# Performance work log

Hardware: AMD Instinct MI355X
Metric: run time of the kernel (lower is better)

## Reference

```python
import jax, jax.numpy as jnp
import numpy as np


def setup_inputs() -> dict:
    key = jax.random.key(0)
    k1, k2, k3, k4, k5 = jax.random.split(key, 5)
    B, C, G, H, W = 2, 64, 4, 64, 64
    CG = C * G            # 256 complex input channels (flattened)
    DQK = max(C // 8, 1)  # 8  query/key channels after gabor pooling
    scale = 1.0 / np.sqrt(CG)
    x = jax.random.normal(k1, (2, B, C, G, H, W), dtype=jnp.float32)
    wq = jax.random.normal(k2, (2, DQK, CG), dtype=jnp.float32) * scale
    wk = jax.random.normal(k3, (2, DQK, CG), dtype=jnp.float32) * scale
    wv = jax.random.normal(k4, (2, CG, CG), dtype=jnp.float32) * scale
    gamma = jax.random.normal(k5, (1,), dtype=jnp.float32) * 0.1
    return {"x": x, "wq": wq, "wk": wk, "wv": wv, "gamma": gamma}


def _cconv1x1(w, xr, xi):
    """Complex 1x1 conv: (wr+i wi)(xr+i xi). w: (2,O,Cin), x: (B,Cin,L)."""
    wr, wi = w[0], w[1]
    yr = jnp.einsum('oc,bcl->bol', wr, xr) - jnp.einsum('oc,bcl->bol', wi, xi)
    yi = jnp.einsum('oc,bcl->bol', wr, xi) + jnp.einsum('oc,bcl->bol', wi, xr)
    return yr, yi


def reference(x, wq, wk, wv, gamma):
    _, B, C, G, H, W = x.shape
    L = H * W
    xr = x[0].reshape(B, C * G, L)
    xi = x[1].reshape(B, C * G, L)
    # complex Q (B,d,L) / K (B,d,L)
    qr, qi = _cconv1x1(wq, xr, xi)
    kr, ki = _cconv1x1(wk, xr, xi)
    # energy = Q^H-free complex bmm: energy[b,l,m] = sum_d q[b,d,l] * k[b,d,m]
    er = jnp.einsum('bdl,bdm->blm', qr, kr) - jnp.einsum('bdl,bdm->blm', qi, ki)
    ei = jnp.einsum('bdl,bdm->blm', qr, ki) + jnp.einsum('bdl,bdm->blm', qi, kr)
    # magnitude-squared softmax over last axis -> real attention (B,L,L)
    att = jax.nn.softmax(er * er + ei * ei, axis=-1)
    # complex V (B,CG,L); out[b,c,m] = sum_l v[b,c,l] * att[b,m,l]
    vr, vi = _cconv1x1(wv, xr, xi)
    out_r = jnp.einsum('bcl,bml->bcm', vr, att)
    out_i = jnp.einsum('bcl,bml->bcm', vi, att)
    out = jnp.stack([out_r, out_i]).reshape(2, B, C, G, H, W)
    return gamma * out + x
```

## Files before the change

### kernel.cpp

```cpp
#include <hip/hip_runtime.h>
#include <cstdint>

constexpr int Bc  = 2;
constexpr int CGc = 256;
constexpr int Dc  = 8;
constexpr int Lc  = 4096;

typedef __attribute__((ext_vector_type(8))) short short8;
typedef __attribute__((ext_vector_type(4))) float floatx4;

__device__ inline unsigned short f2bf(float f) {
  union { float f; unsigned u; } v; v.f = f;
  unsigned r = v.u + 0x7fffu + ((v.u >> 16) & 1u);
  return (unsigned short)(r >> 16);
}
__device__ inline float bf2f(unsigned short h) {
  return __uint_as_float((unsigned)h << 16);
}

__global__ __launch_bounds__(256) void init_stats(float* __restrict__ p) {
  p[blockIdx.x * 256 + threadIdx.x] = 0.f;
}

__global__ __launch_bounds__(256) void wcat_pack(const float* __restrict__ wv,
                                                 unsigned short* __restrict__ Wcat) {
  const int i  = blockIdx.x * 256 + threadIdx.x;
  const int cc = i >> 9, k = i & 511;
  const int co = cc >> 8, c = cc & 255, ci = k >> 8, cin = k & 255;
  const float wr = wv[(size_t)c * CGc + cin];
  const float wi = wv[(size_t)(CGc + c) * CGc + cin];
  const float val = co == 0 ? (ci == 0 ? wr : -wi) : (ci == 0 ? wi : wr);
  Wcat[i] = f2bf(val);
}

__global__ __launch_bounds__(256) void xT_pack(const float* __restrict__ x,
                                               unsigned short* __restrict__ Xlk) {
  __shared__ float xs[64][65];
  const int tid = threadIdx.x;
  const int b   = blockIdx.z;
  const int l0  = blockIdx.x * 64;
  const int c0  = blockIdx.y * 64;
  const int lt  = tid & 63, r4 = tid >> 6;
#pragma unroll
  for (int p = 0; p < 16; ++p) {
    const int row  = p * 4 + r4;
    const int cin2 = c0 + row;
    const int comp = cin2 >> 8, cin = cin2 & 255;
    xs[row][lt] = x[((size_t)(comp * Bc + b) * CGc + cin) * Lc + l0 + lt];
  }
  __syncthreads();
#pragma unroll
  for (int p = 0; p < 16; ++p) {
    const int lr = p * 4 + r4;
    Xlk[((size_t)b * Lc + l0 + lr) * 512 + c0 + lt] = f2bf(xs[lt][lr]);
  }
}

__global__ __launch_bounds__(256) void qk_proj(const float* __restrict__ x,
                                               const float* __restrict__ wq,
                                               const float* __restrict__ wk,
                                               float* __restrict__ qout,
                                               float* __restrict__ kout) {
  __shared__ float ws[4 * Dc * CGc];
  const int tid = threadIdx.x;
  const int b   = blockIdx.y;
  for (int i = tid; i < 2 * Dc * CGc; i += 256) {
    ws[i]                 = wq[i];
    ws[2 * Dc * CGc + i]  = wk[i];
  }
  __syncthreads();
  const int d  = tid >> 5;
  const int ml = tid & 31;
  const int m  = blockIdx.x * 32 + ml;
  const float* xr = x + ((size_t)(0 * Bc + b) * CGc) * Lc + m;
  const float* xi = x + ((size_t)(1 * Bc + b) * CGc) * Lc + m;
  const float* wqr = ws + d * CGc;
  const float* wqi = ws + (Dc + d) * CGc;
  const float* wkr = ws + 2 * Dc * CGc + d * CGc;
  const float* wki = ws + 2 * Dc * CGc + (Dc + d) * CGc;
  float qer = 0.f, qei = 0.f, ker = 0.f, kei = 0.f;
#pragma unroll 4
  for (int cin = 0; cin < CGc; ++cin) {
    const float vr = xr[(size_t)cin * Lc];
    const float vi = xi[(size_t)cin * Lc];
    const float a1 = wqr[cin], b1 = wqi[cin];
    qer = fmaf(a1, vr, qer); qer = fmaf(-b1, vi, qer);
    qei = fmaf(a1, vi, qei); qei = fmaf(b1, vr, qei);
    const float a2 = wkr[cin], b2 = wki[cin];
    ker = fmaf(a2, vr, ker); ker = fmaf(-b2, vi, ker);
    kei = fmaf(a2, vi, kei); kei = fmaf(b2, vr, kei);
  }
  float* qp = qout + ((size_t)b * Lc + m) * 16;
  qp[d]     = qer;
  qp[8 + d] = qei;
  float* kp = kout + ((size_t)b * Lc + m) * 16;
  kp[d]     = ker;
  kp[8 + d] = kei;
}

__global__ __launch_bounds__(256) void qk_pack(const float* __restrict__ q,
                                               const float* __restrict__ k,
                                               unsigned short* __restrict__ Qcat,
                                               unsigned short* __restrict__ K1hi,
                                               unsigned short* __restrict__ K1lo,
                                               unsigned short* __restrict__ K2hi,
                                               unsigned short* __restrict__ K2lo) {
  const int r = blockIdx.x * 256 + threadIdx.x;
  {
    const float* qp = q + (size_t)r * 16;
    unsigned u[16];
#pragma unroll
    for (int t = 0; t < 8; ++t) {
      const float v0 = qp[2 * t], v1 = qp[2 * t + 1];
      const unsigned short h0 = f2bf(v0), h1 = f2bf(v1);
      u[t] = (unsigned)h0 | ((unsigned)h1 << 16);
      const unsigned short l0 = f2bf(v0 - bf2f(h0));
      const unsigned short l1 = f2bf(v1 - bf2f(h1));
      u[8 + t] = (unsigned)l0 | ((unsigned)l1 << 16);
    }
    uint4* dst = (uint4*)(Qcat + (size_t)r * 32);
    dst[0] = make_uint4(u[0], u[1], u[2], u[3]);
    dst[1] = make_uint4(u[4], u[5], u[6], u[7]);
    dst[2] = make_uint4(u[8], u[9], u[10], u[11]);
    dst[3] = make_uint4(u[12], u[13], u[14], u[15]);
  }
  {
    const float* kp = k + (size_t)r * 16;
    float k1[16], k2[16];
#pragma unroll
    for (int d = 0; d < 8; ++d) {
      const float kr = kp[d], ki = kp[8 + d];
      k1[d] = kr;  k1[8 + d] = -ki;
      k2[d] = ki;  k2[8 + d] = kr;
    }
    unsigned uh[8], ul[8];
#pragma unroll
    for (int t = 0; t < 8; ++t) {
      const unsigned short h0 = f2bf(k1[2 * t]), h1 = f2bf(k1[2 * t + 1]);
      uh[t] = (unsigned)h0 | ((unsigned)h1 << 16);
      const unsigned short l0 = f2bf(k1[2 * t] - bf2f(h0));
      const unsigned short l1 = f2bf(k1[2 * t + 1] - bf2f(h1));
      ul[t] = (unsigned)l0 | ((unsigned)l1 << 16);
    }
    uint4* dh = (uint4*)(K1hi + (size_t)r * 16);
    dh[0] = make_uint4(uh[0], uh[1], uh[2], uh[3]);
    dh[1] = make_uint4(uh[4], uh[5], uh[6], uh[7]);
    uint4* dl = (uint4*)(K1lo + (size_t)r * 16);
    dl[0] = make_uint4(ul[0], ul[1], ul[2], ul[3]);
    dl[1] = make_uint4(ul[4], ul[5], ul[6], ul[7]);
#pragma unroll
    for (int t = 0; t < 8; ++t) {
      const unsigned short h0 = f2bf(k2[2 * t]), h1 = f2bf(k2[2 * t + 1]);
      uh[t] = (unsigned)h0 | ((unsigned)h1 << 16);
      const unsigned short l0 = f2bf(k2[2 * t] - bf2f(h0));
      const unsigned short l1 = f2bf(k2[2 * t + 1] - bf2f(h1));
      ul[t] = (unsigned)l0 | ((unsigned)l1 << 16);
    }
    uint4* dh2 = (uint4*)(K2hi + (size_t)r * 16);
    dh2[0] = make_uint4(uh[0], uh[1], uh[2], uh[3]);
    dh2[1] = make_uint4(uh[4], uh[5], uh[6], uh[7]);
    uint4* dl2 = (uint4*)(K2lo + (size_t)r * 16);
    dl2[0] = make_uint4(ul[0], ul[1], ul[2], ul[3]);
    dl2[1] = make_uint4(ul[4], ul[5], ul[6], ul[7]);
  }
}

__global__ __launch_bounds__(256) void v_gemm(const unsigned short* __restrict__ Wcat,
                                              const unsigned short* __restrict__ Xlk,
                                              unsigned short* __restrict__ vbf) {
  __shared__ short As[128 * 64];
  __shared__ short Bs[64 * 64];
  const int tid  = threadIdx.x;
  const int b    = blockIdx.z;
  const int cc0  = blockIdx.x * 128;
  const int l0   = blockIdx.y * 64;
  const int wid  = tid >> 6, lane = tid & 63;
  const int wcc  = (wid >> 1) * 64;
  const int wl   = (wid & 1) * 32;
  const int lrow = lane & 15, quad = lane >> 4;
  floatx4 acc[4][2] = {};
  const unsigned short* wsrc = Wcat + (size_t)cc0 * 512;
  const unsigned short* xsrc = Xlk + ((size_t)b * Lc + l0) * 512;
  int s_off[4], g_off[4];
#pragma unroll
  for (int r = 0; r < 4; ++r) {
    const int idx = r * 256 + tid;
    const int row = idx >> 3, ch = idx & 7;
    s_off[r] = row * 64 + (ch ^ (row & 7)) * 8;
    g_off[r] = row * 512 + ch * 8;
  }
  short8 ar[4], br[2];
#pragma unroll
  for (int r = 0; r < 4; ++r) ar[r] = *(const short8*)(wsrc + g_off[r]);
#pragma unroll
  for (int r = 0; r < 2; ++r) br[r] = *(const short8*)(xsrc + g_off[r]);
  for (int k0 = 0; k0 < 512; k0 += 64) {
    __syncthreads();
#pragma unroll
    for (int r = 0; r < 4; ++r) *(short8*)&As[s_off[r]] = ar[r];
#pragma unroll
    for (int r = 0; r < 2; ++r) *(short8*)&Bs[s_off[r]] = br[r];
    __syncthreads();
    if (k0 + 64 < 512) {
#pragma unroll
      for (int r = 0; r < 4; ++r) ar[r] = *(const short8*)(wsrc + g_off[r] + k0 + 64);
#pragma unroll
      for (int r = 0; r < 2; ++r) br[r] = *(const short8*)(xsrc + g_off[r] + k0 + 64);
    }
#pragma unroll
    for (int kk = 0; kk < 64; kk += 32) {
      const int cb = kk >> 3;
      short8 af[4], bf[2];
#pragma unroll
      for (int i = 0; i < 4; ++i)
        af[i] = *(const short8*)&As[(wcc + i * 16 + lrow) * 64 +
                                    ((cb + quad) ^ (lrow & 7)) * 8];
#pragma unroll
      for (int j = 0; j < 2; ++j)
        bf[j] = *(const short8*)&Bs[(wl + j * 16 + lrow) * 64 +
                                    ((cb + quad) ^ (lrow & 7)) * 8];
#pragma unroll
      for (int i = 0; i < 4; ++i)
#pragma unroll
        for (int j = 0; j < 2; ++j)
          acc[i][j] = __builtin_amdgcn_mfma_f32_16x16x32_bf16(af[i], bf[j], acc[i][j], 0, 0, 0);
    }
  }
#pragma unroll
  for (int i = 0; i < 4; ++i) {
    const int ccb = cc0 + wcc + i * 16 + quad * 4;
#pragma unroll
    for (int j = 0; j < 2; ++j) {
      const int l = l0 + wl + j * 16 + lrow;
#pragma unroll
      for (int rg = 0; rg < 4; ++rg)
        vbf[((size_t)b * 512 + ccb + rg) * Lc + l] = f2bf(acc[i][j][rg]);
    }
  }
}

__global__ __launch_bounds__(256) void e_max(const unsigned short* __restrict__ Qcat,
                                             const unsigned short* __restrict__ K1hi,
                                             const unsigned short* __restrict__ K2hi,
                                             float* __restrict__ Mrow) {
  const int tid  = threadIdx.x;
  const int w    = tid >> 6, lane = tid & 63;
  const int lrow = lane & 15, quad = lane >> 4, qsel = quad & 1;
  const int b    = blockIdx.z;
  const int m16  = blockIdx.x * 64 + w * 16;
  const int lbeg = blockIdx.y * 512;
  const size_t kb = (size_t)b * Lc;
  const short8 afrag = *(const short8*)(Qcat + (kb + m16 + lrow) * 32 + quad * 8);
  float mx[4] = {0.f, 0.f, 0.f, 0.f};
  for (int l0 = lbeg; l0 < lbeg + 512; l0 += 16) {
    const size_t l = kb + l0 + lrow;
    const short8 b1h = *(const short8*)(K1hi + l * 16 + qsel * 8);
    const short8 b2h = *(const short8*)(K2hi + l * 16 + qsel * 8);
    const floatx4 er = __builtin_amdgcn_mfma_f32_16x16x32_bf16(afrag, b1h, (floatx4){0.f, 0.f, 0.f, 0.f}, 0, 0, 0);
    const floatx4 ei = __builtin_amdgcn_mfma_f32_16x16x32_bf16(afrag, b2h, (floatx4){0.f, 0.f, 0.f, 0.f}, 0, 0, 0);
#pragma unroll
    for (int r = 0; r < 4; ++r) {
      float e = er[r] * er[r];
      e = fmaf(ei[r], ei[r], e);
      mx[r] = fmaxf(mx[r], e);
    }
  }
#pragma unroll
  for (int r = 0; r < 4; ++r) {
    float v = mx[r];
#pragma unroll
    for (int off = 1; off < 16; off <<= 1) v = fmaxf(v, __shfl_xor(v, off));
    if (lrow == 0)
      atomicMax((unsigned*)&Mrow[kb + m16 + quad * 4 + r], __float_as_uint(v));
  }
}

__global__ __launch_bounds__(256) void e_exp(const unsigned short* __restrict__ Qcat,
                                             const unsigned short* __restrict__ K1hi,
                                             const unsigned short* __restrict__ K1lo,
                                             const unsigned short* __restrict__ K2hi,
                                             const unsigned short* __restrict__ K2lo,
                                             const float* __restrict__ Mrow,
                                             unsigned short* __restrict__ att,
                                             float* __restrict__ Ssum) {
  const int tid  = threadIdx.x;
  const int w    = tid >> 6, lane = tid & 63;
  const int lrow = lane & 15, quad = lane >> 4, qsel = quad & 1;
  const int b    = blockIdx.z;
  const int m16  = blockIdx.x * 64 + w * 16;
  const int lbeg = blockIdx.y * 512;
  const size_t kb = (size_t)b * Lc;
  const short8 afrag = *(const short8*)(Qcat + (kb + m16 + lrow) * 32 + quad * 8);
  float Mv[4], sum[4] = {};
#pragma unroll
  for (int r = 0; r < 4; ++r) Mv[r] = Mrow[kb + m16 + quad * 4 + r];
  for (int l0 = lbeg; l0 < lbeg + 512; l0 += 16) {
    const size_t l = kb + l0 + lrow;
    const short8 b1h = *(const short8*)(K1hi + l * 16 + qsel * 8);
    const short8 b1l = *(const short8*)(K1lo + l * 16 + qsel * 8);
    const short8 b2h = *(const short8*)(K2hi + l * 16 + qsel * 8);
    const short8 b2l = *(const short8*)(K2lo + l * 16 + qsel * 8);
    floatx4 er = __builtin_amdgcn_mfma_f32_16x16x32_bf16(afrag, b1l, (floatx4){0.f, 0.f, 0.f, 0.f}, 0, 0, 0);
    er = __builtin_amdgcn_mfma_f32_16x16x32_bf16(afrag, b1h, er, 0, 0, 0);
    floatx4 ei = __builtin_amdgcn_mfma_f32_16x16x32_bf16(afrag, b2l, (floatx4){0.f, 0.f, 0.f, 0.f}, 0, 0, 0);
    ei = __builtin_amdgcn_mfma_f32_16x16x32_bf16(afrag, b2h, ei, 0, 0, 0);
#pragma unroll
    for (int r = 0; r < 4; ++r) {
      float e = er[r] * er[r];
      e = fmaf(ei[r], ei[r], e);
      const float wgt = __expf(e - Mv[r]);
      sum[r] += wgt;
      att[(kb + m16 + quad * 4 + r) * Lc + l0 + lrow] = f2bf(wgt);
    }
  }
#pragma unroll
  for (int r = 0; r < 4; ++r) {
    float v = sum[r];
#pragma unroll
    for (int off = 1; off < 16; off <<= 1) v += __shfl_xor(v, off);
    if (lrow == 0) atomicAdd(&Ssum[kb + m16 + quad * 4 + r], v);
  }
}

__device__ __forceinline__ void pv_stage(const unsigned short* __restrict__ vsrc,
                                         const unsigned short* __restrict__ asrc,
                                         short* lds_buf, int k0, int wid, int lane) {
  const int rsub = lane >> 3;
  const int ch   = (lane & 7) ^ rsub;
#pragma unroll
  for (int t = 0; t < 4; ++t) {
    const int q    = wid * 4 + t;
    const int tile = q >> 4;
    const int j    = q & 15;
    const int row  = j * 8 + rsub;
    const unsigned short* g =
        (tile == 0 ? vsrc : asrc) + (size_t)row * Lc + k0 + ch * 8;
    short* l = lds_buf + tile * 8192 + j * 512;
    __builtin_amdgcn_global_load_lds(
        (const __attribute__((address_space(1))) void*)g,
        (__attribute__((address_space(3))) void*)l, 16, 0, 0);
  }
}

__device__ __forceinline__ void pv_compute32(const short* __restrict__ As,
                                             const short* __restrict__ Bs,
                                             int cb, int wcc, int wm, int lrow, int quad,
                                             floatx4 (&acc)[4][4]) {
  short8 af[4], bf[4];
#pragma unroll
  for (int i = 0; i < 4; ++i)
    af[i] = *(const short8*)&As[(wcc + i * 16 + lrow) * 64 +
                                ((cb + quad) ^ (lrow & 7)) * 8];
#pragma unroll
  for (int j = 0; j < 4; ++j)
    bf[j] = *(const short8*)&Bs[(wm + j * 16 + lrow) * 64 +
                                ((cb + quad) ^ (lrow & 7)) * 8];
#pragma unroll
  for (int i = 0; i < 4; ++i)
#pragma unroll
    for (int j = 0; j < 4; ++j)
      acc[i][j] = __builtin_amdgcn_mfma_f32_16x16x32_bf16(af[i], bf[j], acc[i][j], 0, 0, 0);
}

__global__ __launch_bounds__(512, 2) void pv_gemm(const unsigned short* __restrict__ v,
                                                  const unsigned short* __restrict__ att,
                                                  const float* __restrict__ Ssum,
                                                  const float* __restrict__ x,
                                                  const float* __restrict__ gamma,
                                                  float* __restrict__ out) {
  extern __shared__ short smem[];
  const int flat = blockIdx.x;
  const int swz  = (flat & 7) * 32 + (flat >> 3);
  const int b    = swz >> 7;
  const int rem  = swz & 127;
  const int m0   = (rem >> 2) * 128;
  const int cc0  = (rem & 3) * 128;
  const int tid  = threadIdx.x;
  const int wid  = tid >> 6, lane = tid & 63;
  const int g    = wid >> 2;
  const int w4   = wid & 3;
  const int wcc  = (w4 >> 1) * 64;
  const int wm   = (w4 & 1) * 64;
  const int lrow = lane & 15, quad = lane >> 4;
  const int cb   = g * 4;
  floatx4 acc[4][4] = {};
  const unsigned short* vsrc = v   + ((size_t)b * 512 + cc0) * Lc;
  const unsigned short* asrc = att + ((size_t)b * Lc + m0) * Lc;
  pv_stage(vsrc, asrc, smem,          0, wid, lane);
  pv_stage(vsrc, asrc, smem + 16384, 64, wid, lane);
  int cur = 0;
  for (int p = 0; p < 64; ++p) {
    if (p + 2 < 64) {
      const int nxt = cur + 2 > 2 ? cur - 1 : cur + 2;
      pv_stage(vsrc, asrc, smem + nxt * 16384, (p + 2) * 64, wid, lane);
      asm volatile("s_waitcnt vmcnt(8)" ::: "memory");
    } else if (p + 1 < 64) {
      asm volatile("s_waitcnt vmcnt(4)" ::: "memory");
    } else {
      asm volatile("s_waitcnt vmcnt(0)" ::: "memory");
    }
    __builtin_amdgcn_s_barrier();
    __builtin_amdgcn_sched_barrier(0);
    pv_compute32(smem + cur * 16384, smem + cur * 16384 + 8192,
                 cb, wcc, wm, lrow, quad, acc);
    __builtin_amdgcn_sched_barrier(0);
    __builtin_amdgcn_s_barrier();
    cur = cur + 1 > 2 ? 0 : cur + 1;
  }
  float* red = (float*)smem;
  if (g == 1) {
#pragma unroll
    for (int i = 0; i < 4; ++i)
#pragma unroll
      for (int j = 0; j < 4; ++j) {
        const int tq = i * 4 + j;
        *(floatx4*)&red[((w4 * 64 + lane) * 16 + (tq ^ (lane & 15))) * 4] = acc[i][j];
      }
  }
  __syncthreads();
  if (g == 0) {
#pragma unroll
    for (int i = 0; i < 4; ++i)
#pragma unroll
      for (int j = 0; j < 4; ++j) {
        const int tq = i * 4 + j;
        const floatx4 o = *(const floatx4*)&red[((w4 * 64 + lane) * 16 + (tq ^ (lane & 15))) * 4];
        acc[i][j] += o;
      }
    const float gm = gamma[0];
    float svj[4];
#pragma unroll
    for (int j = 0; j < 4; ++j)
      svj[j] = gm / Ssum[(size_t)b * Lc + m0 + wm + j * 16 + lrow];
#pragma unroll
    for (int i = 0; i < 4; ++i) {
      const int ccb = cc0 + wcc + i * 16 + quad * 4;
#pragma unroll
      for (int j = 0; j < 4; ++j) {
        const int m = m0 + wm + j * 16 + lrow;
#pragma unroll
        for (int rg = 0; rg < 4; ++rg) {
          const int cc   = ccb + rg;
          const int comp = cc >> 8, c = cc & 255;
          const size_t idx = (((size_t)comp * Bc + b) * CGc + c) * Lc + m;
          out[idx] = svj[j] * acc[i][j][rg] + x[idx];
        }
      }
    }
  }
}

extern "C" void kernel_launch(void* const* d_in, const int* in_sizes, int n_in,
                              void* d_out, int out_size, void* d_ws, size_t ws_size,
                              hipStream_t stream) {
  const float* x     = (const float*)d_in[0];
  const float* wq    = (const float*)d_in[1];
  const float* wk    = (const float*)d_in[2];
  const float* wv    = (const float*)d_in[3];
  const float* gamma = (const float*)d_in[4];
  float* out = (float*)d_out;

  float* q    = (float*)d_ws;
  float* kk   = q    + (size_t)Bc * Lc * 16;
  float* Mrow = kk   + (size_t)Bc * Lc * 16;
  float* Ssum = Mrow + (size_t)Bc * Lc;
  unsigned short* vbf  = (unsigned short*)(Ssum + (size_t)Bc * Lc);
  unsigned short* att  = vbf + (size_t)Bc * 512 * Lc;
  unsigned short* Xlk  = att;
  unsigned short* Qcat = att + (size_t)Bc * Lc * Lc;
  unsigned short* K1hi = Qcat + (size_t)Bc * Lc * 32;
  unsigned short* K1lo = K1hi + (size_t)Bc * Lc * 16;
  unsigned short* K2hi = K1lo + (size_t)Bc * Lc * 16;
  unsigned short* K2lo = K2hi + (size_t)Bc * Lc * 16;
  unsigned short* Wcat = K2lo + (size_t)Bc * Lc * 16;

  init_stats<<<dim3((2 * Bc * Lc) / 256), 256, 0, stream>>>(Mrow);
  wcat_pack<<<dim3((512 * 512) / 256), 256, 0, stream>>>(wv, Wcat);
  qk_proj<<<dim3(Lc / 32, Bc), 256, 0, stream>>>(x, wq, wk, q, kk);
  qk_pack<<<dim3((Bc * Lc) / 256), 256, 0, stream>>>(q, kk, Qcat, K1hi, K1lo, K2hi, K2lo);
  xT_pack<<<dim3(Lc / 64, 8, Bc), 256, 0, stream>>>(x, Xlk);
  v_gemm<<<dim3(512 / 128, Lc / 64, Bc), 256, 0, stream>>>(Wcat, Xlk, vbf);
  e_max<<<dim3(Lc / 64, 8, Bc), 256, 0, stream>>>(Qcat, K1hi, K2hi, Mrow);
  e_exp<<<dim3(Lc / 64, 8, Bc), 256, 0, stream>>>(Qcat, K1hi, K1lo, K2hi, K2lo, Mrow, att, Ssum);
  pv_gemm<<<dim3(256), 512, 3 * 16384 * sizeof(short), stream>>>(vbf, att, Ssum, x, gamma, out);
}
```

Measured before the change: 202.5 us.

## Fuse setup kernels and drop a barrier from the PV pipeline loop

Merges the stats-zeroing and weight-packing kernels into one launch, and fuses the QK projection with its bf16 hi/lo packing through shared memory so the fp32 Q/K intermediates are no longer written to and reread from global memory. In the PV GEMM loop, the wait and barrier now come before issuing the next stage's loads. This lets one barrier per iteration both publish the current buffer and protect the buffer being overwritten, removing the trailing barrier. The goal is fewer launches and fewer synchronizations, at the cost of a tighter vmcnt wait (4 instead of 8), which leaves fewer loads in flight during the wait.

```diff
diff --git a/kernel.cpp b/kernel.cpp
--- a/kernel.cpp
+++ b/kernel.cpp
@@ -18,13 +18,15 @@
   return __uint_as_float((unsigned)h << 16);
 }
 
-__global__ __launch_bounds__(256) void init_stats(float* __restrict__ p) {
-  p[blockIdx.x * 256 + threadIdx.x] = 0.f;
-}
-
-__global__ __launch_bounds__(256) void wcat_pack(const float* __restrict__ wv,
+__global__ __launch_bounds__(256) void init_wcat(float* __restrict__ stats,
+                                                 const float* __restrict__ wv,
                                                  unsigned short* __restrict__ Wcat) {
-  const int i  = blockIdx.x * 256 + threadIdx.x;
+  const int bx = blockIdx.x;
+  if (bx < 64) {
+    stats[bx * 256 + threadIdx.x] = 0.f;
+    return;
+  }
+  const int i  = (bx - 64) * 256 + threadIdx.x;
   const int cc = i >> 9, k = i & 511;
   const int co = cc >> 8, c = cc & 255, ci = k >> 8, cin = k & 255;
   const float wr = wv[(size_t)c * CGc + cin];
@@ -56,12 +58,17 @@
   }
 }
 
-__global__ __launch_bounds__(256) void qk_proj(const float* __restrict__ x,
-                                               const float* __restrict__ wq,
-                                               const float* __restrict__ wk,
-                                               float* __restrict__ qout,
-                                               float* __restrict__ kout) {
+__global__ __launch_bounds__(256) void qk_projpack(const float* __restrict__ x,
+                                                   const float* __restrict__ wq,
+                                                   const float* __restrict__ wk,
+                                                   unsigned short* __restrict__ Qcat,
+                                                   unsigned short* __restrict__ K1hi,
+                                                   unsigned short* __restrict__ K1lo,
+                                                   unsigned short* __restrict__ K2hi,
+                                                   unsigned short* __restrict__ K2lo) {
   __shared__ float ws[4 * Dc * CGc];
+  __shared__ float qs[32][16];
+  __shared__ float ks[32][16];
   const int tid = threadIdx.x;
   const int b   = blockIdx.y;
   for (int i = tid; i < 2 * Dc * CGc; i += 256) {
@@ -90,78 +97,55 @@
     ker = fmaf(a2, vr, ker); ker = fmaf(-b2, vi, ker);
     kei = fmaf(a2, vi, kei); kei = fmaf(b2, vr, kei);
   }
-  float* qp = qout + ((size_t)b * Lc + m) * 16;
-  qp[d]     = qer;
-  qp[8 + d] = qei;
-  float* kp = kout + ((size_t)b * Lc + m) * 16;
-  kp[d]     = ker;
-  kp[8 + d] = kei;
-}
-
-__global__ __launch_bounds__(256) void qk_pack(const float* __restrict__ q,
-                                               const float* __restrict__ k,
-                                               unsigned short* __restrict__ Qcat,
-                                               unsigned short* __restrict__ K1hi,
-                                               unsigned short* __restrict__ K1lo,
-                                               unsigned short* __restrict__ K2hi,
-                                               unsigned short* __restrict__ K2lo) {
-  const int r = blockIdx.x * 256 + threadIdx.x;
-  {
-    const float* qp = q + (size_t)r * 16;
-    unsigned u[16];
+  qs[ml][d] = qer;  qs[ml][8 + d] = qei;
+  ks[ml][d] = ker;  ks[ml][8 + d] = kei;
+  __syncthreads();
+  const int part = tid >> 5;
+  const int rl   = tid & 31;
+  const size_t r = (size_t)b * Lc + blockIdx.x * 32 + rl;
+  if (part < 2) {
+    unsigned u[8];
 #pragma unroll
     for (int t = 0; t < 8; ++t) {
-      const float v0 = qp[2 * t], v1 = qp[2 * t + 1];
+      const float v0 = qs[rl][2 * t], v1 = qs[rl][2 * t + 1];
       const unsigned short h0 = f2bf(v0), h1 = f2bf(v1);
-      u[t] = (unsigned)h0 | ((unsigned)h1 << 16);
-      const unsigned short l0 = f2bf(v0 - bf2f(h0));
-      const unsigned short l1 = f2bf(v1 - bf2f(h1));
-      u[8 + t] = (unsigned)l0 | ((unsigned)l1 << 16);
-    }
-    uint4* dst = (uint4*)(Qcat + (size_t)r * 32);
+      if (part == 0) {
+        u[t] = (unsigned)h0 | ((unsigned)h1 << 16);
+      } else {
+        const unsigned short l0 = f2bf(v0 - bf2f(h0));
+        const unsigned short l1 = f2bf(v1 - bf2f(h1));
+        u[t] = (unsigned)l0 | ((unsigned)l1 << 16);
+      }
+    }
+    uint4* dst = (uint4*)(Qcat + r * 32 + part * 16);
     dst[0] = make_uint4(u[0], u[1], u[2], u[3]);
     dst[1] = make_uint4(u[4], u[5], u[6], u[7]);
-    dst[2] = make_uint4(u[8], u[9], u[10], u[11]);
-    dst[3] = make_uint4(u[12], u[13], u[14], u[15]);
-  }
-  {
-    const float* kp = k + (size_t)r * 16;
-    float k1[16], k2[16];
-#pragma unroll
-    for (int d = 0; d < 8; ++d) {
-      const float kr = kp[d], ki = kp[8 + d];
-      k1[d] = kr;  k1[8 + d] = -ki;
-      k2[d] = ki;  k2[8 + d] = kr;
-    }
-    unsigned uh[8], ul[8];
+  } else if (part < 6) {
+    float kv[16];
+    if (part < 4) {
+#pragma unroll
+      for (int e = 0; e < 8; ++e) { kv[e] = ks[rl][e]; kv[8 + e] = -ks[rl][8 + e]; }
+    } else {
+#pragma unroll
+      for (int e = 0; e < 8; ++e) { kv[e] = ks[rl][8 + e]; kv[8 + e] = ks[rl][e]; }
+    }
+    const int lo = part & 1;
+    unsigned u[8];
 #pragma unroll
     for (int t = 0; t < 8; ++t) {
-      const unsigned short h0 = f2bf(k1[2 * t]), h1 = f2bf(k1[2 * t + 1]);
-      uh[t] = (unsigned)h0 | ((unsigned)h1 << 16);
-      const unsigned short l0 = f2bf(k1[2 * t] - bf2f(h0));
-      const unsigned short l1 = f2bf(k1[2 * t + 1] - bf2f(h1));
-      ul[t] = (unsigned)l0 | ((unsigned)l1 << 16);
-    }
-    uint4* dh = (uint4*)(K1hi + (size_t)r * 16);
-    dh[0] = make_uint4(uh[0], uh[1], uh[2], uh[3]);
-    dh[1] = make_uint4(uh[4], uh[5], uh[6], uh[7]);
-    uint4* dl = (uint4*)(K1lo + (size_t)r * 16);
-    dl[0] = make_uint4(ul[0], ul[1], ul[2], ul[3]);
-    dl[1] = make_uint4(ul[4], ul[5], ul[6], ul[7]);
-#pragma unroll
-    for (int t = 0; t < 8; ++t) {
-      const unsigned short h0 = f2bf(k2[2 * t]), h1 = f2bf(k2[2 * t + 1]);
-      uh[t] = (unsigned)h0 | ((unsigned)h1 << 16);
-      const unsigned short l0 = f2bf(k2[2 * t] - bf2f(h0));
-      const unsigned short l1 = f2bf(k2[2 * t + 1] - bf2f(h1));
-      ul[t] = (unsigned)l0 | ((unsigned)l1 << 16);
-    }
-    uint4* dh2 = (uint4*)(K2hi + (size_t)r * 16);
-    dh2[0] = make_uint4(uh[0], uh[1], uh[2], uh[3]);
-    dh2[1] = make_uint4(uh[4], uh[5], uh[6], uh[7]);
-    uint4* dl2 = (uint4*)(K2lo + (size_t)r * 16);
-    dl2[0] = make_uint4(ul[0], ul[1], ul[2], ul[3]);
-    dl2[1] = make_uint4(ul[4], ul[5], ul[6], ul[7]);
+      const unsigned short h0 = f2bf(kv[2 * t]), h1 = f2bf(kv[2 * t + 1]);
+      if (!lo) {
+        u[t] = (unsigned)h0 | ((unsigned)h1 << 16);
+      } else {
+        const unsigned short l0 = f2bf(kv[2 * t] - bf2f(h0));
+        const unsigned short l1 = f2bf(kv[2 * t + 1] - bf2f(h1));
+        u[t] = (unsigned)l0 | ((unsigned)l1 << 16);
+      }
+    }
+    unsigned short* base = part < 4 ? (lo ? K1lo : K1hi) : (lo ? K2lo : K2hi);
+    uint4* dst = (uint4*)(base + r * 16);
+    dst[0] = make_uint4(u[0], u[1], u[2], u[3]);
+    dst[1] = make_uint4(u[4], u[5], u[6], u[7]);
   }
 }
 
@@ -390,23 +374,24 @@
   pv_stage(vsrc, asrc, smem + 16384, 64, wid, lane);
   int cur = 0;
   for (int p = 0; p < 64; ++p) {
+    if (p < 63) {
+      asm volatile("s_waitcnt vmcnt(4)" ::: "memory");
+    } else {
+      asm volatile("s_waitcnt vmcnt(0)" ::: "memory");
+    }
+    __builtin_amdgcn_s_barrier();
+    __builtin_amdgcn_sched_barrier(0);
     if (p + 2 < 64) {
       const int nxt = cur + 2 > 2 ? cur - 1 : cur + 2;
       pv_stage(vsrc, asrc, smem + nxt * 16384, (p + 2) * 64, wid, lane);
-      asm volatile("s_waitcnt vmcnt(8)" ::: "memory");
-    } else if (p + 1 < 64) {
-      asm volatile("s_waitcnt vmcnt(4)" ::: "memory");
-    } else {
-      asm volatile("s_waitcnt vmcnt(0)" ::: "memory");
-    }
-    __builtin_amdgcn_s_barrier();
+    }
     __builtin_amdgcn_sched_barrier(0);
     pv_compute32(smem + cur * 16384, smem + cur * 16384 + 8192,
                  cb, wcc, wm, lrow, quad, acc);
     __builtin_amdgcn_sched_barrier(0);
-    __builtin_amdgcn_s_barrier();
     cur = cur + 1 > 2 ? 0 : cur + 1;
   }
+  __syncthreads();
   float* red = (float*)smem;
   if (g == 1) {
 #pragma unroll
@@ -474,10 +459,8 @@
   unsigned short* K2lo = K2hi + (size_t)Bc * Lc * 16;
   unsigned short* Wcat = K2lo + (size_t)Bc * Lc * 16;
 
-  init_stats<<<dim3((2 * Bc * Lc) / 256), 256, 0, stream>>>(Mrow);
-  wcat_pack<<<dim3((512 * 512) / 256), 256, 0, stream>>>(wv, Wcat);
-  qk_proj<<<dim3(Lc / 32, Bc), 256, 0, stream>>>(x, wq, wk, q, kk);
-  qk_pack<<<dim3((Bc * Lc) / 256), 256, 0, stream>>>(q, kk, Qcat, K1hi, K1lo, K2hi, K2lo);
+  init_wcat<<<dim3(64 + 1024), 256, 0, stream>>>(Mrow, wv, Wcat);
+  qk_projpack<<<dim3(Lc / 32, Bc), 256, 0, stream>>>(x, wq, wk, Qcat, K1hi, K1lo, K2hi, K2lo);
   xT_pack<<<dim3(Lc / 64, 8, Bc), 256, 0, stream>>>(x, Xlk);
   v_gemm<<<dim3(512 / 128, Lc / 64, Bc), 256, 0, stream>>>(Wcat, Xlk, vbf);
   e_max<<<dim3(Lc / 64, 8, Bc), 256, 0, stream>>>(Qcat, K1hi, K2hi, Mrow);
```

Result: faster. 194.6 us (-3.9%).
